# Optimization experiments

Hardware: AMD Instinct MI355X
Metric: run time of the kernel (lower is better)

## Reference

```python
import jax, jax.numpy as jnp
import numpy as np
jax.config.update("jax_enable_x64", True)


def setup_inputs() -> dict:
    key = jax.random.key(0)
    k0, k1, k2 = jax.random.split(key, 3)
    B, T, D, H, NX = 4, 4096, 1024, 32, 12
    NV = D // H  # 32
    x = jax.random.normal(k0, (B, T, D), jnp.float32)
    wx = jax.random.normal(k1, (D, H * NX), jnp.float32) / np.sqrt(D).astype(np.float32)
    wv = jax.random.normal(k2, (D, H * NV), jnp.float32) / np.sqrt(D).astype(np.float32)
    emb0 = jnp.full((D,), -1e-5, jnp.float32)
    emb1 = jnp.full((D,), +1e-5, jnp.float32)
    return {"x": x, "wx": wx, "wv": wv, "emb0": emb0, "emb1": emb1,
            "num_x_bits": NX, "num_v_bits": NV}


def _pack_bits(logits, B, T, H, nb):
    # (logits > 0) -> [B,T,H,nb] -> [B,H,T,nb] -> packed int64 keys [B,H,T]
    bits = (logits > 0).reshape(B, T, H, nb).transpose(0, 2, 1, 3).astype(jnp.int64)
    r = jnp.arange(nb, dtype=jnp.int64)
    return jnp.sum(bits << r, axis=-1)


def _rosa_scan(keys, vals, num_x_bits):
    # Sequential associative-memory automaton, vectorized over (B, H) streams.
    # State: table[b,h,key] (2^num_x_bits slots, init 0).
    # Per step t: y_t = table[key_t] (read), then table[key_t] = v_t (write).
    B, H, T = keys.shape
    table0 = jnp.zeros((B, H, 1 << num_x_bits), jnp.int64)
    bi = jnp.arange(B)[:, None]
    hi = jnp.arange(H)[None, :]

    def step(table, kv):
        k, v = kv  # [B,H]
        y = table[bi, hi, k]
        return table.at[bi, hi, k].set(v), y

    _, ys = jax.lax.scan(step, table0,
                         (keys.transpose(2, 0, 1), vals.transpose(2, 0, 1)))
    return ys.transpose(1, 2, 0)  # [B,H,T]


def reference(x, wx, wv, emb0, emb1, num_x_bits, num_v_bits):
    B, T, D = x.shape
    H = D // num_v_bits
    xx = x @ wx  # [B,T,H*nx]
    xv = x @ wv  # [B,T,H*nv]
    kx = _pack_bits(xx, B, T, H, num_x_bits)  # [B,H,T] int keys
    kv = _pack_bits(xv, B, T, H, num_v_bits)  # [B,H,T] int values
    y = _rosa_scan(kx, kv, num_x_bits)        # [B,H,T] recalled values
    rv = jnp.arange(num_v_bits, dtype=jnp.int64)
    m = ((y[..., None] >> rv) & 1).astype(bool)      # [B,H,T,nv]
    m = m.transpose(0, 2, 1, 3).reshape(B, T, D)      # [B,T,D]
    return jnp.where(m, emb1, emb0)
```

## Files before the change

kernel.cpp:

```cpp
#include <hip/hip_runtime.h>
#include <stdint.h>

#define B_ 4
#define T_ 4096
#define D_ 1024
#define H_ 32
#define NX_ 12
#define NV_ 32
#define NCOL 1408
#define TAU 2e-4f
#define BITW 88

typedef __attribute__((ext_vector_type(8))) short short8v;
typedef __attribute__((ext_vector_type(4))) float floatx4;

static __device__ __forceinline__ unsigned short bf16_rne(float f) {
  unsigned u = __float_as_uint(f);
  return (unsigned short)((u + 0x7FFFu + ((u >> 16) & 1u)) >> 16);
}
static __device__ __forceinline__ float bf16_to_f32(unsigned short h) {
  return __uint_as_float(((unsigned)h) << 16);
}


__global__ __launch_bounds__(256) void wsplit_kernel(
    const float* __restrict__ wx, const float* __restrict__ wv,
    unsigned short* __restrict__ Wt_hi, unsigned short* __restrict__ Wt_lo)
{
  __shared__ float tile[64][65];
  const int tid = threadIdx.x;
  const int cb = blockIdx.x % (NCOL / 64);
  const int kb = blockIdx.x / (NCOL / 64);
  const int c_local = tid & 63;
  const int c_glob = cb * 64 + c_local;

#pragma unroll
  for (int i = 0; i < 16; ++i) {
    const int k_local = (tid >> 6) + i * 4;
    const int k_glob = kb * 64 + k_local;
    const float v = (c_glob < 384) ? wx[k_glob * 384 + c_glob]
                                   : wv[k_glob * 1024 + (c_glob - 384)];
    tile[k_local][c_local] = v;
  }
  __syncthreads();

#pragma unroll
  for (int i = 0; i < 4; ++i) {
    const int q = (tid >> 6) * 4 + i;
    const int k0 = q * 4;
    const int r = k0 & 31;
    const int g = (r < 16) ? (r >> 2) : ((r - 16) >> 2);
    const int half = (r < 16) ? 0 : 1;
    const int p = g * 8 + half * 4;
    const long dst = (long)c_glob * 1024 + kb * 64 + (k0 & 32) + p;
    ushort4 hv, lv;
    float f0 = tile[k0 + 0][c_local], f1 = tile[k0 + 1][c_local];
    float f2 = tile[k0 + 2][c_local], f3 = tile[k0 + 3][c_local];
    hv.x = bf16_rne(f0); lv.x = bf16_rne(f0 - bf16_to_f32(hv.x));
    hv.y = bf16_rne(f1); lv.y = bf16_rne(f1 - bf16_to_f32(hv.y));
    hv.z = bf16_rne(f2); lv.z = bf16_rne(f2 - bf16_to_f32(hv.z));
    hv.w = bf16_rne(f3); lv.w = bf16_rne(f3 - bf16_to_f32(hv.w));
    *(ushort4*)&Wt_hi[dst] = hv;
    *(ushort4*)&Wt_lo[dst] = lv;
  }
}

__global__ __launch_bounds__(256) void gemm_kernel(
    const float* __restrict__ x,
    const unsigned short* __restrict__ Wt_hi,
    const unsigned short* __restrict__ Wt_lo,
    const float* __restrict__ wx, const float* __restrict__ wv,
    unsigned short* __restrict__ bitmat)
{
  __shared__ unsigned short Ah[4096], Al[4096], Bh[4096], Bl[4096];

  const int tid = threadIdx.x;
  const int wid = tid >> 6, lane = tid & 63;
  const int wr = wid >> 1, wc = wid & 1;
  const int bx = blockIdx.x % 11;
  const int by = blockIdx.x / 11;

  floatx4 acc[4][4];
#pragma unroll
  for (int i = 0; i < 4; ++i)
#pragma unroll
    for (int j = 0; j < 4; ++j) acc[i][j] = (floatx4)0.f;

  const int arow = tid >> 1;
  const int ahalf = tid & 1;

  for (int ks = 0; ks < 32; ++ks) {
    __syncthreads();

    {
      const float4* xp = (const float4*)(x + ((long)(by * 128 + arow)) * 1024
                                           + ks * 32 + ahalf * 16);
      float4 f[4];
#pragma unroll
      for (int g = 0; g < 4; ++g) f[g] = xp[g];
#pragma unroll
      for (int g = 0; g < 4; ++g) {
        const int sl = g ^ ((arow >> 1) & 3);
        const int idx = arow * 32 + sl * 8 + ahalf * 4;
        ushort4 hv, lv;
        hv.x = bf16_rne(f[g].x); lv.x = bf16_rne(f[g].x - bf16_to_f32(hv.x));
        hv.y = bf16_rne(f[g].y); lv.y = bf16_rne(f[g].y - bf16_to_f32(hv.y));
        hv.z = bf16_rne(f[g].z); lv.z = bf16_rne(f[g].z - bf16_to_f32(hv.z));
        hv.w = bf16_rne(f[g].w); lv.w = bf16_rne(f[g].w - bf16_to_f32(hv.w));
        *(ushort4*)&Ah[idx] = hv;
        *(ushort4*)&Al[idx] = lv;
      }
    }

#pragma unroll
    for (int i = 0; i < 2; ++i) {
      const int c = wid * 64 + i * 256 + lane;
      const int row = c >> 2, sl = c & 3;
      const int g = sl ^ ((row >> 1) & 3);
      const long src = ((long)(bx * 128 + row)) * 1024 + ks * 32 + g * 8;
      __builtin_amdgcn_global_load_lds(
          (const __attribute__((address_space(1))) unsigned int*)(Wt_hi + src),
          (__attribute__((address_space(3))) unsigned int*)&Bh[c * 8], 16, 0, 0);
      __builtin_amdgcn_global_load_lds(
          (const __attribute__((address_space(1))) unsigned int*)(Wt_lo + src),
          (__attribute__((address_space(3))) unsigned int*)&Bl[c * 8], 16, 0, 0);
    }

    __syncthreads();

    short8v ah[4], al[4], bh[4], bl[4];
    const int g = lane >> 4;
#pragma unroll
    for (int mi = 0; mi < 4; ++mi) {
      const int row = wr * 64 + mi * 16 + (lane & 15);
      const int off = row * 32 + (g ^ ((row >> 1) & 3)) * 8;
      ah[mi] = *(const short8v*)&Ah[off];
      al[mi] = *(const short8v*)&Al[off];
    }
#pragma unroll
    for (int nj = 0; nj < 4; ++nj) {
      const int row = wc * 64 + nj * 16 + (lane & 15);
      const int off = row * 32 + (g ^ ((row >> 1) & 3)) * 8;
      bh[nj] = *(const short8v*)&Bh[off];
      bl[nj] = *(const short8v*)&Bl[off];
    }
#pragma unroll
    for (int mi = 0; mi < 4; ++mi)
#pragma unroll
      for (int nj = 0; nj < 4; ++nj) {
        acc[mi][nj] = __builtin_amdgcn_mfma_f32_16x16x32_bf16(
            ah[mi], bh[nj], acc[mi][nj], 0, 0, 0);
        acc[mi][nj] = __builtin_amdgcn_mfma_f32_16x16x32_bf16(
            ah[mi], bl[nj], acc[mi][nj], 0, 0, 0);
        acc[mi][nj] = __builtin_amdgcn_mfma_f32_16x16x32_bf16(
            al[mi], bh[nj], acc[mi][nj], 0, 0, 0);
      }
  }

#pragma unroll
  for (int mi = 0; mi < 4; ++mi)
#pragma unroll
    for (int nj = 0; nj < 4; ++nj) {
      const int colg = bx * 128 + wc * 64 + nj * 16 + (lane & 15);
      const int rowbase = by * 128 + wr * 64 + mi * 16 + ((lane >> 4) * 4);
      const int col16 = bx * 8 + wc * 4 + nj;
#pragma unroll
      for (int r = 0; r < 4; ++r) {
        const float v = acc[mi][nj][r];
        bool pos = v > 0.f;
        if (fabsf(v) < TAU) {
          const float* xr = x + (long)(rowbase + r) * 1024;
          const float* wp; int ldw;
          if (colg < 384) { wp = wx + colg; ldw = 384; }
          else            { wp = wv + (colg - 384); ldw = 1024; }
          double s0 = 0, s1 = 0, s2 = 0, s3 = 0;
          for (int d = 0; d < 1024; d += 4) {
            s0 = fma((double)xr[d + 0], (double)wp[(long)(d + 0) * ldw], s0);
            s1 = fma((double)xr[d + 1], (double)wp[(long)(d + 1) * ldw], s1);
            s2 = fma((double)xr[d + 2], (double)wp[(long)(d + 2) * ldw], s2);
            s3 = fma((double)xr[d + 3], (double)wp[(long)(d + 3) * ldw], s3);
          }
          pos = ((s0 + s1) + (s2 + s3)) > 0.0;
        }
        const unsigned long long mask = __ballot(pos);
        if ((lane & 15) == 0)
          bitmat[(long)(rowbase + r) * BITW + col16] =
              (unsigned short)((mask >> (lane & 48)) & 0xFFFFull);
      }
    }
}

__global__ __launch_bounds__(256) void pack_kernel(
    const unsigned short* __restrict__ bitmat,
    unsigned short* __restrict__ kxg, unsigned int* __restrict__ kvg)
{
  const int gid = blockIdx.x * 256 + threadIdx.x;
  const int row = gid >> 5;
  const int h = gid & 31;
  const int b = row >> 12, t = row & (T_ - 1);
  const unsigned short* bp = bitmat + (long)row * BITW;
  const int bitpos = h * NX_;
  const int w0 = bitpos >> 4, off = bitpos & 15;
  const unsigned int v32 = (unsigned int)bp[w0] | ((unsigned int)bp[w0 + 1] << 16);
  const unsigned int key = (v32 >> off) & 0xFFFu;
  const unsigned int val = (unsigned int)bp[24 + 2 * h] |
                           ((unsigned int)bp[25 + 2 * h] << 16);
  const long sidx = ((long)b * H_ + h) * T_ + t;
  kxg[sidx] = (unsigned short)key;
  kvg[sidx] = val;
}

#define CH 1024
#define UNR 16

__global__ __launch_bounds__(256) void scan_kernel(
    const unsigned short* __restrict__ kxg,
    const unsigned int* __restrict__ kvg,
    unsigned int* __restrict__ yg)
{
  __shared__ unsigned int table[1 << NX_];
  __shared__ unsigned int kbuf[CH], vbuf[CH], ybuf[CH];
  const int tid = threadIdx.x;
  const long base = (long)blockIdx.x * T_;

#pragma unroll
  for (int i = 0; i < (1 << NX_) / 256; ++i) table[tid + 256 * i] = 0u;

  for (int c = 0; c < T_ / CH; ++c) {
    __syncthreads();
#pragma unroll
    for (int i = 0; i < CH / 256; ++i) {
      kbuf[tid + 256 * i] = kxg[base + c * CH + tid + 256 * i];
      vbuf[tid + 256 * i] = kvg[base + c * CH + tid + 256 * i];
    }
    __syncthreads();
    if (tid == 0) {
      for (int i = 0; i < CH; i += UNR) {
        unsigned int k[UNR], v[UNR], y[UNR];
#pragma unroll
        for (int u = 0; u < UNR; ++u) { k[u] = kbuf[i + u]; v[u] = vbuf[i + u]; }
#pragma unroll
        for (int u = 0; u < UNR; ++u) { y[u] = table[k[u]]; table[k[u]] = v[u]; }
#pragma unroll
        for (int u = 0; u < UNR; ++u) ybuf[i + u] = y[u];
      }
    }
    __syncthreads();
#pragma unroll
    for (int i = 0; i < CH / 256; ++i)
      yg[base + c * CH + tid + 256 * i] = ybuf[tid + 256 * i];
  }
}

__global__ __launch_bounds__(256) void out_kernel(
    const unsigned int* __restrict__ yg,
    const float* __restrict__ e0, const float* __restrict__ e1,
    float* __restrict__ out)
{
  const int tid = threadIdx.x;
  const int bt = blockIdx.x;
  const int b = bt >> 12, t = bt & (T_ - 1);
  const int h = tid >> 3;
  const unsigned int y = yg[((long)b * H_ + h) * T_ + t];
  const int d0 = tid * 4;
  const int vsh = (tid & 7) * 4;
  float4 o;
  o.x = ((y >> (vsh + 0)) & 1) ? e1[d0 + 0] : e0[d0 + 0];
  o.y = ((y >> (vsh + 1)) & 1) ? e1[d0 + 1] : e0[d0 + 1];
  o.z = ((y >> (vsh + 2)) & 1) ? e1[d0 + 2] : e0[d0 + 2];
  o.w = ((y >> (vsh + 3)) & 1) ? e1[d0 + 3] : e0[d0 + 3];
  *(float4*)&out[(long)bt * D_ + d0] = o;
}

extern "C" void kernel_launch(void* const* d_in, const int* in_sizes, int n_in,
                              void* d_out, int out_size, void* d_ws, size_t ws_size,
                              hipStream_t stream)
{
  const float* x  = (const float*)d_in[0];
  const float* wx = (const float*)d_in[1];
  const float* wv = (const float*)d_in[2];
  const float* e0 = (const float*)d_in[3];
  const float* e1 = (const float*)d_in[4];

  char* ws = (char*)d_ws;
  const size_t MB = 1u << 20;
  unsigned short* Wt_hi  = (unsigned short*)(ws + 0 * MB);
  unsigned short* Wt_lo  = (unsigned short*)(ws + 3 * MB);
  unsigned short* bitmat = (unsigned short*)(ws + 6 * MB);
  unsigned short* kxg    = (unsigned short*)(ws + 9 * MB);
  unsigned int*   kvg    = (unsigned int*)  (ws + 10 * MB);
  unsigned int*   yg     = (unsigned int*)  (ws + 12 * MB);
  float* out = (float*)d_out;

  hipLaunchKernelGGL(wsplit_kernel, dim3((NCOL / 64) * 16), dim3(256), 0, stream,
                     wx, wv, Wt_hi, Wt_lo);
  hipLaunchKernelGGL(gemm_kernel, dim3(11 * 128), dim3(256), 0, stream,
                     x, Wt_hi, Wt_lo, wx, wv, bitmat);
  hipLaunchKernelGGL(pack_kernel, dim3(2048), dim3(256), 0, stream,
                     bitmat, kxg, kvg);
  hipLaunchKernelGGL(scan_kernel, dim3(B_ * H_), dim3(256), 0, stream,
                     kxg, kvg, yg);
  hipLaunchKernelGGL(out_kernel, dim3(B_ * T_), dim3(256), 0, stream,
                     yg, e0, e1, out);
}
```

Measured before the change: 905.3 us.

## Double-buffer GEMM LDS tiles and remap blocks across XCDs

The split-bf16 GEMM now keeps two LDS buffers. Each iteration converts and stores the next A tile from registers prefetched two steps ahead, and issues the next B global-to-LDS loads, while running MFMAs on the current tile. This leaves one barrier per iteration instead of two and is meant to hide global-load latency. The block index is also remapped so consecutive blocks on each XCD share output tiles, and launch bounds now request two blocks per CU. The cost is twice the LDS footprint (64 KB per block) and extra register pressure from the prefetched A data.

```diff
diff --git a/kernel.cpp b/kernel.cpp
--- a/kernel.cpp
+++ b/kernel.cpp
@@ -65,20 +65,38 @@
   }
 }
 
-__global__ __launch_bounds__(256) void gemm_kernel(
+__device__ __forceinline__ void a_write(unsigned short* AhB, unsigned short* AlB,
+                                        int arow, int ahalf, const float4* f)
+{
+#pragma unroll
+  for (int g = 0; g < 4; ++g) {
+    const int sl = g ^ ((arow >> 1) & 3);
+    const int idx = arow * 32 + sl * 8 + ahalf * 4;
+    ushort4 hv, lv;
+    hv.x = bf16_rne(f[g].x); lv.x = bf16_rne(f[g].x - bf16_to_f32(hv.x));
+    hv.y = bf16_rne(f[g].y); lv.y = bf16_rne(f[g].y - bf16_to_f32(hv.y));
+    hv.z = bf16_rne(f[g].z); lv.z = bf16_rne(f[g].z - bf16_to_f32(hv.z));
+    hv.w = bf16_rne(f[g].w); lv.w = bf16_rne(f[g].w - bf16_to_f32(hv.w));
+    *(ushort4*)&AhB[idx] = hv;
+    *(ushort4*)&AlB[idx] = lv;
+  }
+}
+
+__global__ __launch_bounds__(256, 2) void gemm_kernel(
     const float* __restrict__ x,
     const unsigned short* __restrict__ Wt_hi,
     const unsigned short* __restrict__ Wt_lo,
     const float* __restrict__ wx, const float* __restrict__ wv,
     unsigned short* __restrict__ bitmat)
 {
-  __shared__ unsigned short Ah[4096], Al[4096], Bh[4096], Bl[4096];
+  __shared__ unsigned short Ah[2][4096], Al[2][4096], Bh[2][4096], Bl[2][4096];
 
   const int tid = threadIdx.x;
   const int wid = tid >> 6, lane = tid & 63;
   const int wr = wid >> 1, wc = wid & 1;
-  const int bx = blockIdx.x % 11;
-  const int by = blockIdx.x / 11;
+  const int sw = (blockIdx.x & 7) * 176 + (blockIdx.x >> 3);
+  const int bx = sw % 11;
+  const int by = sw / 11;
 
   floatx4 acc[4][4];
 #pragma unroll
@@ -88,45 +106,55 @@
 
   const int arow = tid >> 1;
   const int ahalf = tid & 1;
+  const float4* xbase = (const float4*)(x + ((long)(by * 128 + arow)) * 1024);
+
+  int b_c[2]; long b_src0[2];
+#pragma unroll
+  for (int i = 0; i < 2; ++i) {
+    const int c = wid * 64 + i * 256 + lane;
+    const int row = c >> 2, sl = c & 3;
+    const int g = sl ^ ((row >> 1) & 3);
+    b_c[i] = c;
+    b_src0[i] = ((long)(bx * 128 + row)) * 1024 + g * 8;
+  }
+
+#define STAGE_B(buf, ks)                                                      \
+  {                                                                           \
+    _Pragma("unroll")                                                         \
+    for (int i = 0; i < 2; ++i) {                                             \
+      const long src = b_src0[i] + (ks) * 32;                                 \
+      __builtin_amdgcn_global_load_lds(                                       \
+          (const __attribute__((address_space(1))) unsigned int*)(Wt_hi + src),\
+          (__attribute__((address_space(3))) unsigned int*)&Bh[buf][b_c[i] * 8],\
+          16, 0, 0);                                                          \
+      __builtin_amdgcn_global_load_lds(                                       \
+          (const __attribute__((address_space(1))) unsigned int*)(Wt_lo + src),\
+          (__attribute__((address_space(3))) unsigned int*)&Bl[buf][b_c[i] * 8],\
+          16, 0, 0);                                                          \
+    }                                                                         \
+  }
+
+  float4 fA[4], fN[4];
+#pragma unroll
+  for (int g = 0; g < 4; ++g) fA[g] = xbase[ahalf * 4 + g];
+  a_write(Ah[0], Al[0], arow, ahalf, fA);
+  STAGE_B(0, 0)
+#pragma unroll
+  for (int g = 0; g < 4; ++g) fN[g] = xbase[8 + ahalf * 4 + g];
+  __syncthreads();
 
   for (int ks = 0; ks < 32; ++ks) {
-    __syncthreads();
-
-    {
-      const float4* xp = (const float4*)(x + ((long)(by * 128 + arow)) * 1024
-                                           + ks * 32 + ahalf * 16);
-      float4 f[4];
-#pragma unroll
-      for (int g = 0; g < 4; ++g) f[g] = xp[g];
-#pragma unroll
-      for (int g = 0; g < 4; ++g) {
-        const int sl = g ^ ((arow >> 1) & 3);
-        const int idx = arow * 32 + sl * 8 + ahalf * 4;
-        ushort4 hv, lv;
-        hv.x = bf16_rne(f[g].x); lv.x = bf16_rne(f[g].x - bf16_to_f32(hv.x));
-        hv.y = bf16_rne(f[g].y); lv.y = bf16_rne(f[g].y - bf16_to_f32(hv.y));
-        hv.z = bf16_rne(f[g].z); lv.z = bf16_rne(f[g].z - bf16_to_f32(hv.z));
-        hv.w = bf16_rne(f[g].w); lv.w = bf16_rne(f[g].w - bf16_to_f32(hv.w));
-        *(ushort4*)&Ah[idx] = hv;
-        *(ushort4*)&Al[idx] = lv;
+    const int cur = ks & 1;
+
+    if (ks < 31) {
+      a_write(Ah[cur ^ 1], Al[cur ^ 1], arow, ahalf, fN);
+      STAGE_B(cur ^ 1, ks + 1)
+      if (ks < 30) {
+#pragma unroll
+        for (int g = 0; g < 4; ++g)
+          fN[g] = xbase[(ks + 2) * 8 + ahalf * 4 + g];
       }
     }
-
-#pragma unroll
-    for (int i = 0; i < 2; ++i) {
-      const int c = wid * 64 + i * 256 + lane;
-      const int row = c >> 2, sl = c & 3;
-      const int g = sl ^ ((row >> 1) & 3);
-      const long src = ((long)(bx * 128 + row)) * 1024 + ks * 32 + g * 8;
-      __builtin_amdgcn_global_load_lds(
-          (const __attribute__((address_space(1))) unsigned int*)(Wt_hi + src),
-          (__attribute__((address_space(3))) unsigned int*)&Bh[c * 8], 16, 0, 0);
-      __builtin_amdgcn_global_load_lds(
-          (const __attribute__((address_space(1))) unsigned int*)(Wt_lo + src),
-          (__attribute__((address_space(3))) unsigned int*)&Bl[c * 8], 16, 0, 0);
-    }
-
-    __syncthreads();
 
     short8v ah[4], al[4], bh[4], bl[4];
     const int g = lane >> 4;
@@ -134,15 +162,15 @@
     for (int mi = 0; mi < 4; ++mi) {
       const int row = wr * 64 + mi * 16 + (lane & 15);
       const int off = row * 32 + (g ^ ((row >> 1) & 3)) * 8;
-      ah[mi] = *(const short8v*)&Ah[off];
-      al[mi] = *(const short8v*)&Al[off];
+      ah[mi] = *(const short8v*)&Ah[cur][off];
+      al[mi] = *(const short8v*)&Al[cur][off];
     }
 #pragma unroll
     for (int nj = 0; nj < 4; ++nj) {
       const int row = wc * 64 + nj * 16 + (lane & 15);
       const int off = row * 32 + (g ^ ((row >> 1) & 3)) * 8;
-      bh[nj] = *(const short8v*)&Bh[off];
-      bl[nj] = *(const short8v*)&Bl[off];
+      bh[nj] = *(const short8v*)&Bh[cur][off];
+      bl[nj] = *(const short8v*)&Bl[cur][off];
     }
 #pragma unroll
     for (int mi = 0; mi < 4; ++mi)
@@ -155,6 +183,8 @@
         acc[mi][nj] = __builtin_amdgcn_mfma_f32_16x16x32_bf16(
             al[mi], bh[nj], acc[mi][nj], 0, 0, 0);
       }
+
+    __syncthreads();
   }
 
 #pragma unroll
```

After: 878.2 us. -3.0%, faster.

## Load GEMM operands directly into registers with fragment-ordered weights and double buffering

Applied to the files above, without the earlier changes.

The weight split kernel now writes hi/lo bf16 weights into one buffer laid out in MFMA fragment order, so each lane can load its B operand straight from global memory. The GEMM drops shared memory and barriers and loads A (fp32 x) and B fragments directly into registers. It double-buffers the loads across two k-steps, splits x into hi/lo bf16 in registers, and adds a block-index swizzle plus an occupancy hint. This targets LDS traffic and sync stalls, at the cost of more registers and uncoalesced or redundant global reads of x across the two column-warps.

```diff
diff --git a/kernel.cpp b/kernel.cpp
--- a/kernel.cpp
+++ b/kernel.cpp
@@ -25,7 +25,7 @@
 
 __global__ __launch_bounds__(256) void wsplit_kernel(
     const float* __restrict__ wx, const float* __restrict__ wv,
-    unsigned short* __restrict__ Wt_hi, unsigned short* __restrict__ Wt_lo)
+    unsigned short* __restrict__ WT)
 {
   __shared__ float tile[64][65];
   const int tid = threadIdx.x;
@@ -48,11 +48,13 @@
   for (int i = 0; i < 4; ++i) {
     const int q = (tid >> 6) * 4 + i;
     const int k0 = q * 4;
+    const int ks32 = kb * 2 + (k0 >> 5);
     const int r = k0 & 31;
     const int g = (r < 16) ? (r >> 2) : ((r - 16) >> 2);
     const int half = (r < 16) ? 0 : 1;
-    const int p = g * 8 + half * 4;
-    const long dst = (long)c_glob * 1024 + kb * 64 + (k0 & 32) + p;
+    const int lane = g * 16 + (c_glob & 15);
+    const int ct = c_glob >> 4;
+    const long base = ((long)ks32 * 88 + ct) * 1024 + lane * 8 + half * 4;
     ushort4 hv, lv;
     float f0 = tile[k0 + 0][c_local], f1 = tile[k0 + 1][c_local];
     float f2 = tile[k0 + 2][c_local], f3 = tile[k0 + 3][c_local];
@@ -60,25 +62,28 @@
     hv.y = bf16_rne(f1); lv.y = bf16_rne(f1 - bf16_to_f32(hv.y));
     hv.z = bf16_rne(f2); lv.z = bf16_rne(f2 - bf16_to_f32(hv.z));
     hv.w = bf16_rne(f3); lv.w = bf16_rne(f3 - bf16_to_f32(hv.w));
-    *(ushort4*)&Wt_hi[dst] = hv;
-    *(ushort4*)&Wt_lo[dst] = lv;
-  }
-}
-
-__global__ __launch_bounds__(256) void gemm_kernel(
+    *(ushort4*)&WT[base] = hv;
+    *(ushort4*)&WT[base + 512] = lv;
+  }
+}
+
+__global__ __launch_bounds__(256, 2) void gemm_kernel(
     const float* __restrict__ x,
-    const unsigned short* __restrict__ Wt_hi,
-    const unsigned short* __restrict__ Wt_lo,
+    const unsigned short* __restrict__ WT,
     const float* __restrict__ wx, const float* __restrict__ wv,
     unsigned short* __restrict__ bitmat)
 {
-  __shared__ unsigned short Ah[4096], Al[4096], Bh[4096], Bl[4096];
-
   const int tid = threadIdx.x;
   const int wid = tid >> 6, lane = tid & 63;
   const int wr = wid >> 1, wc = wid & 1;
-  const int bx = blockIdx.x % 11;
-  const int by = blockIdx.x / 11;
+  const int sw = (blockIdx.x & 7) * 176 + (blockIdx.x >> 3);
+  const int bx = sw % 11;
+  const int by = sw / 11;
+
+  const int ln15 = lane & 15, g = lane >> 4;
+  const int g4 = g * 4;
+  const int ct0 = bx * 8 + wc * 4;
+  const float* xA = x + (size_t)(by * 128 + wr * 64 + ln15) * 1024;
 
   floatx4 acc[4][4];
 #pragma unroll
@@ -86,75 +91,74 @@
 #pragma unroll
     for (int j = 0; j < 4; ++j) acc[i][j] = (floatx4)0.f;
 
-  const int arow = tid >> 1;
-  const int ahalf = tid & 1;
-
-  for (int ks = 0; ks < 32; ++ks) {
-    __syncthreads();
-
-    {
-      const float4* xp = (const float4*)(x + ((long)(by * 128 + arow)) * 1024
-                                           + ks * 32 + ahalf * 16);
-      float4 f[4];
-#pragma unroll
-      for (int g = 0; g < 4; ++g) f[g] = xp[g];
-#pragma unroll
-      for (int g = 0; g < 4; ++g) {
-        const int sl = g ^ ((arow >> 1) & 3);
-        const int idx = arow * 32 + sl * 8 + ahalf * 4;
-        ushort4 hv, lv;
-        hv.x = bf16_rne(f[g].x); lv.x = bf16_rne(f[g].x - bf16_to_f32(hv.x));
-        hv.y = bf16_rne(f[g].y); lv.y = bf16_rne(f[g].y - bf16_to_f32(hv.y));
-        hv.z = bf16_rne(f[g].z); lv.z = bf16_rne(f[g].z - bf16_to_f32(hv.z));
-        hv.w = bf16_rne(f[g].w); lv.w = bf16_rne(f[g].w - bf16_to_f32(hv.w));
-        *(ushort4*)&Ah[idx] = hv;
-        *(ushort4*)&Al[idx] = lv;
-      }
-    }
-
-#pragma unroll
-    for (int i = 0; i < 2; ++i) {
-      const int c = wid * 64 + i * 256 + lane;
-      const int row = c >> 2, sl = c & 3;
-      const int g = sl ^ ((row >> 1) & 3);
-      const long src = ((long)(bx * 128 + row)) * 1024 + ks * 32 + g * 8;
-      __builtin_amdgcn_global_load_lds(
-          (const __attribute__((address_space(1))) unsigned int*)(Wt_hi + src),
-          (__attribute__((address_space(3))) unsigned int*)&Bh[c * 8], 16, 0, 0);
-      __builtin_amdgcn_global_load_lds(
-          (const __attribute__((address_space(1))) unsigned int*)(Wt_lo + src),
-          (__attribute__((address_space(3))) unsigned int*)&Bl[c * 8], 16, 0, 0);
-    }
-
-    __syncthreads();
-
-    short8v ah[4], al[4], bh[4], bl[4];
-    const int g = lane >> 4;
-#pragma unroll
-    for (int mi = 0; mi < 4; ++mi) {
-      const int row = wr * 64 + mi * 16 + (lane & 15);
-      const int off = row * 32 + (g ^ ((row >> 1) & 3)) * 8;
-      ah[mi] = *(const short8v*)&Ah[off];
-      al[mi] = *(const short8v*)&Al[off];
-    }
-#pragma unroll
-    for (int nj = 0; nj < 4; ++nj) {
-      const int row = wc * 64 + nj * 16 + (lane & 15);
-      const int off = row * 32 + (g ^ ((row >> 1) & 3)) * 8;
-      bh[nj] = *(const short8v*)&Bh[off];
-      bl[nj] = *(const short8v*)&Bl[off];
-    }
-#pragma unroll
-    for (int mi = 0; mi < 4; ++mi)
-#pragma unroll
-      for (int nj = 0; nj < 4; ++nj) {
-        acc[mi][nj] = __builtin_amdgcn_mfma_f32_16x16x32_bf16(
-            ah[mi], bh[nj], acc[mi][nj], 0, 0, 0);
-        acc[mi][nj] = __builtin_amdgcn_mfma_f32_16x16x32_bf16(
-            ah[mi], bl[nj], acc[mi][nj], 0, 0, 0);
-        acc[mi][nj] = __builtin_amdgcn_mfma_f32_16x16x32_bf16(
-            al[mi], bh[nj], acc[mi][nj], 0, 0, 0);
-      }
+  float4 Aa0[4], Ab0[4], Aa1[4], Ab1[4];
+  short8v Bh0[4], Bl0[4], Bh1[4], Bl1[4];
+
+#define LOAD_A(DA, DB, KS)                                                    \
+  {                                                                           \
+    _Pragma("unroll")                                                         \
+    for (int mi = 0; mi < 4; ++mi) {                                          \
+      const float* xp = xA + (size_t)mi * 16384 + (KS) * 32 + g4;             \
+      DA[mi] = *(const float4*)xp;                                            \
+      DB[mi] = *(const float4*)(xp + 16);                                     \
+    }                                                                         \
+  }
+
+#define LOAD_B(DH, DL, KS)                                                    \
+  {                                                                           \
+    _Pragma("unroll")                                                         \
+    for (int nj = 0; nj < 4; ++nj) {                                          \
+      const unsigned short* wp =                                              \
+          WT + ((size_t)(KS) * 88 + ct0 + nj) * 1024 + lane * 8;              \
+      DH[nj] = *(const short8v*)wp;                                           \
+      DL[nj] = *(const short8v*)(wp + 512);                                   \
+    }                                                                         \
+  }
+
+#define SPLIT1(dst_h, dst_l, f, e)                                            \
+  {                                                                           \
+    const unsigned short hh = bf16_rne(f);                                    \
+    dst_h[e] = (short)hh;                                                     \
+    dst_l[e] = (short)bf16_rne((f)-bf16_to_f32(hh));                          \
+  }
+
+#define COMPUTE(SA, SB, BH, BL)                                               \
+  {                                                                           \
+    short8v ah[4], al[4];                                                     \
+    _Pragma("unroll")                                                         \
+    for (int mi = 0; mi < 4; ++mi) {                                          \
+      SPLIT1(ah[mi], al[mi], SA[mi].x, 0)                                     \
+      SPLIT1(ah[mi], al[mi], SA[mi].y, 1)                                     \
+      SPLIT1(ah[mi], al[mi], SA[mi].z, 2)                                     \
+      SPLIT1(ah[mi], al[mi], SA[mi].w, 3)                                     \
+      SPLIT1(ah[mi], al[mi], SB[mi].x, 4)                                     \
+      SPLIT1(ah[mi], al[mi], SB[mi].y, 5)                                     \
+      SPLIT1(ah[mi], al[mi], SB[mi].z, 6)                                     \
+      SPLIT1(ah[mi], al[mi], SB[mi].w, 7)                                     \
+    }                                                                         \
+    _Pragma("unroll")                                                         \
+    for (int mi = 0; mi < 4; ++mi)                                            \
+      _Pragma("unroll")                                                       \
+      for (int nj = 0; nj < 4; ++nj) {                                        \
+        acc[mi][nj] = __builtin_amdgcn_mfma_f32_16x16x32_bf16(                \
+            ah[mi], BH[nj], acc[mi][nj], 0, 0, 0);                            \
+        acc[mi][nj] = __builtin_amdgcn_mfma_f32_16x16x32_bf16(                \
+            ah[mi], BL[nj], acc[mi][nj], 0, 0, 0);                            \
+        acc[mi][nj] = __builtin_amdgcn_mfma_f32_16x16x32_bf16(                \
+            al[mi], BH[nj], acc[mi][nj], 0, 0, 0);                            \
+      }                                                                       \
+  }
+
+  LOAD_A(Aa0, Ab0, 0)
+  LOAD_B(Bh0, Bl0, 0)
+#pragma unroll 1
+  for (int t = 0; t < 16; ++t) {
+    const int ks = 2 * t;
+    if (t < 15) { LOAD_A(Aa1, Ab1, ks + 1) LOAD_B(Bh1, Bl1, ks + 1) }
+    else        { LOAD_A(Aa1, Ab1, 31)     LOAD_B(Bh1, Bl1, 31) }
+    COMPUTE(Aa0, Ab0, Bh0, Bl0)
+    if (t < 15) { LOAD_A(Aa0, Ab0, ks + 2) LOAD_B(Bh0, Bl0, ks + 2) }
+    COMPUTE(Aa1, Ab1, Bh1, Bl1)
   }
 
 #pragma unroll
@@ -284,8 +288,7 @@
 
   char* ws = (char*)d_ws;
   const size_t MB = 1u << 20;
-  unsigned short* Wt_hi  = (unsigned short*)(ws + 0 * MB);
-  unsigned short* Wt_lo  = (unsigned short*)(ws + 3 * MB);
+  unsigned short* WT     = (unsigned short*)(ws + 0 * MB);
   unsigned short* bitmat = (unsigned short*)(ws + 6 * MB);
   unsigned short* kxg    = (unsigned short*)(ws + 9 * MB);
   unsigned int*   kvg    = (unsigned int*)  (ws + 10 * MB);
@@ -293,9 +296,9 @@
   float* out = (float*)d_out;
 
   hipLaunchKernelGGL(wsplit_kernel, dim3((NCOL / 64) * 16), dim3(256), 0, stream,
-                     wx, wv, Wt_hi, Wt_lo);
+                     wx, wv, WT);
   hipLaunchKernelGGL(gemm_kernel, dim3(11 * 128), dim3(256), 0, stream,
-                     x, Wt_hi, Wt_lo, wx, wv, bitmat);
+                     x, WT, wx, wv, bitmat);
   hipLaunchKernelGGL(pack_kernel, dim3(2048), dim3(256), 0, stream,
                      bitmat, kxg, kvg);
   hipLaunchKernelGGL(scan_kernel, dim3(B_ * H_), dim3(256), 0, stream,
```

Measured after the change: 975.0 us. 1.08x slower.

## Pre-split x and W into MFMA fragment layout, read operands directly from global

Applied to the files above, without the earlier changes.

Adds an xsplit kernel that converts x to bf16 hi/lo pairs stored in MFMA-fragment order, and changes the weight split to emit the same fragment-tiled layout with hi and lo interleaved. The GEMM then drops LDS staging and barriers and loads fragments straight from global memory, with a swizzled block order and launch bounds set for two blocks per SIMD. A fallback GEMM that converts x in registers is used when the workspace is too small. The cost is an extra pass writing 64 MB of bf16 copies of x, and every operand read now goes to global or L2 instead of LDS.

```diff
diff --git a/kernel.cpp b/kernel.cpp
--- a/kernel.cpp
+++ b/kernel.cpp
@@ -25,7 +25,7 @@
 
 __global__ __launch_bounds__(256) void wsplit_kernel(
     const float* __restrict__ wx, const float* __restrict__ wv,
-    unsigned short* __restrict__ Wt_hi, unsigned short* __restrict__ Wt_lo)
+    unsigned short* __restrict__ WT)
 {
   __shared__ float tile[64][65];
   const int tid = threadIdx.x;
@@ -48,11 +48,13 @@
   for (int i = 0; i < 4; ++i) {
     const int q = (tid >> 6) * 4 + i;
     const int k0 = q * 4;
-    const int r = k0 & 31;
-    const int g = (r < 16) ? (r >> 2) : ((r - 16) >> 2);
-    const int half = (r < 16) ? 0 : 1;
-    const int p = g * 8 + half * 4;
-    const long dst = (long)c_glob * 1024 + kb * 64 + (k0 & 32) + p;
+    const int ks32 = kb * 2 + (k0 >> 5);
+    const int kr = k0 & 31;
+    const int half = kr >> 4;
+    const int g = (kr & 15) >> 2;
+    const int lane = g * 16 + (c_glob & 15);
+    const int ct = c_glob >> 4;
+    const long base = ((long)ks32 * 88 + ct) * 1024 + lane * 8 + half * 4;
     ushort4 hv, lv;
     float f0 = tile[k0 + 0][c_local], f1 = tile[k0 + 1][c_local];
     float f2 = tile[k0 + 2][c_local], f3 = tile[k0 + 3][c_local];
@@ -60,25 +62,52 @@
     hv.y = bf16_rne(f1); lv.y = bf16_rne(f1 - bf16_to_f32(hv.y));
     hv.z = bf16_rne(f2); lv.z = bf16_rne(f2 - bf16_to_f32(hv.z));
     hv.w = bf16_rne(f3); lv.w = bf16_rne(f3 - bf16_to_f32(hv.w));
-    *(ushort4*)&Wt_hi[dst] = hv;
-    *(ushort4*)&Wt_lo[dst] = lv;
-  }
-}
-
-__global__ __launch_bounds__(256) void gemm_kernel(
+    *(ushort4*)&WT[base] = hv;
+    *(ushort4*)&WT[base + 512] = lv;
+  }
+}
+
+__global__ __launch_bounds__(256) void xsplit_kernel(
     const float* __restrict__ x,
-    const unsigned short* __restrict__ Wt_hi,
-    const unsigned short* __restrict__ Wt_lo,
+    unsigned short* __restrict__ XTh, unsigned short* __restrict__ XTl)
+{
+  const long q = (long)blockIdx.x * 256 + threadIdx.x;
+  const int row = (int)(q >> 8);
+  const int k0 = ((int)q & 255) * 4;
+  const float4 f = *(const float4*)(x + (long)row * 1024 + k0);
+  const int rt = row >> 4, r15 = row & 15;
+  const int ks = k0 >> 5, kr = k0 & 31;
+  const int half = kr >> 4;
+  const int g = (kr & 15) >> 2;
+  const int lane = g * 16 + r15;
+  const long base = ((long)ks * 1024 + rt) * 512 + lane * 8 + half * 4;
+  ushort4 hv, lv;
+  hv.x = bf16_rne(f.x); lv.x = bf16_rne(f.x - bf16_to_f32(hv.x));
+  hv.y = bf16_rne(f.y); lv.y = bf16_rne(f.y - bf16_to_f32(hv.y));
+  hv.z = bf16_rne(f.z); lv.z = bf16_rne(f.z - bf16_to_f32(hv.z));
+  hv.w = bf16_rne(f.w); lv.w = bf16_rne(f.w - bf16_to_f32(hv.w));
+  *(ushort4*)&XTh[base] = hv;
+  *(ushort4*)&XTl[base] = lv;
+}
+
+__global__ __launch_bounds__(256, 2) void gemm_kernel(
+    const float* __restrict__ x,
+    const unsigned short* __restrict__ XTh,
+    const unsigned short* __restrict__ XTl,
+    const unsigned short* __restrict__ WT,
     const float* __restrict__ wx, const float* __restrict__ wv,
     unsigned short* __restrict__ bitmat)
 {
-  __shared__ unsigned short Ah[4096], Al[4096], Bh[4096], Bl[4096];
-
   const int tid = threadIdx.x;
   const int wid = tid >> 6, lane = tid & 63;
   const int wr = wid >> 1, wc = wid & 1;
-  const int bx = blockIdx.x % 11;
-  const int by = blockIdx.x / 11;
+  const int sw = (blockIdx.x & 7) * 176 + (blockIdx.x >> 3);
+  const int bx = sw % 11;
+  const int by = sw / 11;
+
+  const int rt0 = by * 8 + wr * 4;
+  const int ct0 = bx * 8 + wc * 4;
+  const int l8 = lane * 8;
 
   floatx4 acc[4][4];
 #pragma unroll
@@ -86,63 +115,20 @@
 #pragma unroll
     for (int j = 0; j < 4; ++j) acc[i][j] = (floatx4)0.f;
 
-  const int arow = tid >> 1;
-  const int ahalf = tid & 1;
-
+#pragma unroll 2
   for (int ks = 0; ks < 32; ++ks) {
-    __syncthreads();
-
-    {
-      const float4* xp = (const float4*)(x + ((long)(by * 128 + arow)) * 1024
-                                           + ks * 32 + ahalf * 16);
-      float4 f[4];
-#pragma unroll
-      for (int g = 0; g < 4; ++g) f[g] = xp[g];
-#pragma unroll
-      for (int g = 0; g < 4; ++g) {
-        const int sl = g ^ ((arow >> 1) & 3);
-        const int idx = arow * 32 + sl * 8 + ahalf * 4;
-        ushort4 hv, lv;
-        hv.x = bf16_rne(f[g].x); lv.x = bf16_rne(f[g].x - bf16_to_f32(hv.x));
-        hv.y = bf16_rne(f[g].y); lv.y = bf16_rne(f[g].y - bf16_to_f32(hv.y));
-        hv.z = bf16_rne(f[g].z); lv.z = bf16_rne(f[g].z - bf16_to_f32(hv.z));
-        hv.w = bf16_rne(f[g].w); lv.w = bf16_rne(f[g].w - bf16_to_f32(hv.w));
-        *(ushort4*)&Ah[idx] = hv;
-        *(ushort4*)&Al[idx] = lv;
-      }
-    }
-
-#pragma unroll
-    for (int i = 0; i < 2; ++i) {
-      const int c = wid * 64 + i * 256 + lane;
-      const int row = c >> 2, sl = c & 3;
-      const int g = sl ^ ((row >> 1) & 3);
-      const long src = ((long)(bx * 128 + row)) * 1024 + ks * 32 + g * 8;
-      __builtin_amdgcn_global_load_lds(
-          (const __attribute__((address_space(1))) unsigned int*)(Wt_hi + src),
-          (__attribute__((address_space(3))) unsigned int*)&Bh[c * 8], 16, 0, 0);
-      __builtin_amdgcn_global_load_lds(
-          (const __attribute__((address_space(1))) unsigned int*)(Wt_lo + src),
-          (__attribute__((address_space(3))) unsigned int*)&Bl[c * 8], 16, 0, 0);
-    }
-
-    __syncthreads();
-
     short8v ah[4], al[4], bh[4], bl[4];
-    const int g = lane >> 4;
 #pragma unroll
     for (int mi = 0; mi < 4; ++mi) {
-      const int row = wr * 64 + mi * 16 + (lane & 15);
-      const int off = row * 32 + (g ^ ((row >> 1) & 3)) * 8;
-      ah[mi] = *(const short8v*)&Ah[off];
-      al[mi] = *(const short8v*)&Al[off];
+      const long abase = ((long)ks * 1024 + rt0 + mi) * 512 + l8;
+      ah[mi] = *(const short8v*)&XTh[abase];
+      al[mi] = *(const short8v*)&XTl[abase];
     }
 #pragma unroll
     for (int nj = 0; nj < 4; ++nj) {
-      const int row = wc * 64 + nj * 16 + (lane & 15);
-      const int off = row * 32 + (g ^ ((row >> 1) & 3)) * 8;
-      bh[nj] = *(const short8v*)&Bh[off];
-      bl[nj] = *(const short8v*)&Bl[off];
+      const long wbase = ((long)ks * 88 + ct0 + nj) * 1024 + l8;
+      bh[nj] = *(const short8v*)&WT[wbase];
+      bl[nj] = *(const short8v*)&WT[wbase + 512];
     }
 #pragma unroll
     for (int mi = 0; mi < 4; ++mi)
@@ -190,6 +176,105 @@
     }
 }
 
+__global__ __launch_bounds__(256, 2) void gemm_fb_kernel(
+    const float* __restrict__ x,
+    const unsigned short* __restrict__ WT,
+    const float* __restrict__ wx, const float* __restrict__ wv,
+    unsigned short* __restrict__ bitmat)
+{
+  const int tid = threadIdx.x;
+  const int wid = tid >> 6, lane = tid & 63;
+  const int wr = wid >> 1, wc = wid & 1;
+  const int sw = (blockIdx.x & 7) * 176 + (blockIdx.x >> 3);
+  const int bx = sw % 11;
+  const int by = sw / 11;
+
+  const int ln15 = lane & 15, g = lane >> 4;
+  const int g4 = g * 4;
+  const int ct0 = bx * 8 + wc * 4;
+  const float* xA = x + (size_t)(by * 128 + wr * 64 + ln15) * 1024;
+
+  floatx4 acc[4][4];
+#pragma unroll
+  for (int i = 0; i < 4; ++i)
+#pragma unroll
+    for (int j = 0; j < 4; ++j) acc[i][j] = (floatx4)0.f;
+
+#pragma unroll 1
+  for (int ks = 0; ks < 32; ++ks) {
+    float4 Aa[4], Ab[4];
+    short8v bh[4], bl[4];
+#pragma unroll
+    for (int mi = 0; mi < 4; ++mi) {
+      const float* xp = xA + (size_t)mi * 16384 + ks * 32 + g4;
+      Aa[mi] = *(const float4*)xp;
+      Ab[mi] = *(const float4*)(xp + 16);
+    }
+#pragma unroll
+    for (int nj = 0; nj < 4; ++nj) {
+      const unsigned short* wp =
+          WT + ((size_t)ks * 88 + ct0 + nj) * 1024 + lane * 8;
+      bh[nj] = *(const short8v*)wp;
+      bl[nj] = *(const short8v*)(wp + 512);
+    }
+    short8v ah[4], al[4];
+#pragma unroll
+    for (int mi = 0; mi < 4; ++mi) {
+      const float fe[8] = {Aa[mi].x, Aa[mi].y, Aa[mi].z, Aa[mi].w,
+                           Ab[mi].x, Ab[mi].y, Ab[mi].z, Ab[mi].w};
+#pragma unroll
+      for (int e = 0; e < 8; ++e) {
+        const unsigned short hh = bf16_rne(fe[e]);
+        ah[mi][e] = (short)hh;
+        al[mi][e] = (short)bf16_rne(fe[e] - bf16_to_f32(hh));
+      }
+    }
+#pragma unroll
+    for (int mi = 0; mi < 4; ++mi)
+#pragma unroll
+      for (int nj = 0; nj < 4; ++nj) {
+        acc[mi][nj] = __builtin_amdgcn_mfma_f32_16x16x32_bf16(
+            ah[mi], bh[nj], acc[mi][nj], 0, 0, 0);
+        acc[mi][nj] = __builtin_amdgcn_mfma_f32_16x16x32_bf16(
+            ah[mi], bl[nj], acc[mi][nj], 0, 0, 0);
+        acc[mi][nj] = __builtin_amdgcn_mfma_f32_16x16x32_bf16(
+            al[mi], bh[nj], acc[mi][nj], 0, 0, 0);
+      }
+  }
+
+#pragma unroll
+  for (int mi = 0; mi < 4; ++mi)
+#pragma unroll
+    for (int nj = 0; nj < 4; ++nj) {
+      const int colg = bx * 128 + wc * 64 + nj * 16 + (lane & 15);
+      const int rowbase = by * 128 + wr * 64 + mi * 16 + ((lane >> 4) * 4);
+      const int col16 = bx * 8 + wc * 4 + nj;
+#pragma unroll
+      for (int r = 0; r < 4; ++r) {
+        const float v = acc[mi][nj][r];
+        bool pos = v > 0.f;
+        if (fabsf(v) < TAU) {
+          const float* xr = x + (long)(rowbase + r) * 1024;
+          const float* wp; int ldw;
+          if (colg < 384) { wp = wx + colg; ldw = 384; }
+          else            { wp = wv + (colg - 384); ldw = 1024; }
+          double s0 = 0, s1 = 0, s2 = 0, s3 = 0;
+          for (int d = 0; d < 1024; d += 4) {
+            s0 = fma((double)xr[d + 0], (double)wp[(long)(d + 0) * ldw], s0);
+            s1 = fma((double)xr[d + 1], (double)wp[(long)(d + 1) * ldw], s1);
+            s2 = fma((double)xr[d + 2], (double)wp[(long)(d + 2) * ldw], s2);
+            s3 = fma((double)xr[d + 3], (double)wp[(long)(d + 3) * ldw], s3);
+          }
+          pos = ((s0 + s1) + (s2 + s3)) > 0.0;
+        }
+        const unsigned long long mask = __ballot(pos);
+        if ((lane & 15) == 0)
+          bitmat[(long)(rowbase + r) * BITW + col16] =
+              (unsigned short)((mask >> (lane & 48)) & 0xFFFFull);
+      }
+    }
+}
+
 __global__ __launch_bounds__(256) void pack_kernel(
     const unsigned short* __restrict__ bitmat,
     unsigned short* __restrict__ kxg, unsigned int* __restrict__ kvg)
@@ -284,18 +369,28 @@
 
   char* ws = (char*)d_ws;
   const size_t MB = 1u << 20;
-  unsigned short* Wt_hi  = (unsigned short*)(ws + 0 * MB);
-  unsigned short* Wt_lo  = (unsigned short*)(ws + 3 * MB);
+  unsigned short* WT     = (unsigned short*)(ws + 0 * MB);
   unsigned short* bitmat = (unsigned short*)(ws + 6 * MB);
   unsigned short* kxg    = (unsigned short*)(ws + 9 * MB);
   unsigned int*   kvg    = (unsigned int*)  (ws + 10 * MB);
   unsigned int*   yg     = (unsigned int*)  (ws + 12 * MB);
+  unsigned short* XTh    = (unsigned short*)(ws + 14 * MB);
+  unsigned short* XTl    = (unsigned short*)(ws + 46 * MB);
   float* out = (float*)d_out;
 
+  const bool fast = ws_size >= (size_t)78 * MB;
+
   hipLaunchKernelGGL(wsplit_kernel, dim3((NCOL / 64) * 16), dim3(256), 0, stream,
-                     wx, wv, Wt_hi, Wt_lo);
-  hipLaunchKernelGGL(gemm_kernel, dim3(11 * 128), dim3(256), 0, stream,
-                     x, Wt_hi, Wt_lo, wx, wv, bitmat);
+                     wx, wv, WT);
+  if (fast) {
+    hipLaunchKernelGGL(xsplit_kernel, dim3(16384), dim3(256), 0, stream,
+                       x, XTh, XTl);
+    hipLaunchKernelGGL(gemm_kernel, dim3(11 * 128), dim3(256), 0, stream,
+                       x, XTh, XTl, WT, wx, wv, bitmat);
+  } else {
+    hipLaunchKernelGGL(gemm_fb_kernel, dim3(11 * 128), dim3(256), 0, stream,
+                       x, WT, wx, wv, bitmat);
+  }
   hipLaunchKernelGGL(pack_kernel, dim3(2048), dim3(256), 0, stream,
                      bitmat, kxg, kvg);
   hipLaunchKernelGGL(scan_kernel, dim3(B_ * H_), dim3(256), 0, stream,
```

New measurement: 740.8 us. 1.22x faster.
